# Kernel tuning notes

Hardware: AMD Instinct MI355X
Metric: run time of the kernel (lower is better)

## Reference

```python
import jax, jax.numpy as jnp
import numpy as np


def _bilinear_align_corners(img, H_out, W_out):
    # img: [B, C, h, w] -> [B, C, H_out, W_out], matching F.interpolate(mode='bilinear', align_corners=True)
    b, c, h, w = img.shape
    ys = jnp.linspace(0.0, h - 1.0, H_out)
    xs = jnp.linspace(0.0, w - 1.0, W_out)
    y0 = jnp.floor(ys).astype(jnp.int32)
    x0 = jnp.floor(xs).astype(jnp.int32)
    y1 = jnp.minimum(y0 + 1, h - 1)
    x1 = jnp.minimum(x0 + 1, w - 1)
    wy = (ys - y0)[:, None]          # [H_out, 1]
    wx = (xs - x0)[None, :]          # [1, W_out]

    def gather(yi, xi):
        return img[:, :, yi, :][:, :, :, xi]  # [B, C, H_out, W_out]

    top = gather(y0, x0) * (1.0 - wx) + gather(y0, x1) * wx
    bot = gather(y1, x0) * (1.0 - wx) + gather(y1, x1) * wx
    return top * (1.0 - wy) + bot * wy


def _conv1x1(x, W, b):
    # x: [B, C, H, W_], W: [O, C], b: [O]
    return jnp.einsum('bchw,oc->bohw', x, W) + b[None, :, None, None]


def setup_inputs() -> dict:
    key = jax.random.key(0)
    ks = jax.random.split(key, 9)
    B, C, H, W = 4, 256, 64, 64
    C8 = C // 8
    s_qk = 1.0 / np.sqrt(C)
    return {
        'x': jax.random.normal(ks[0], (B, C, H, W), dtype=jnp.float32),
        'guiding_map0': jax.random.normal(ks[1], (B, 1, 32, 32), dtype=jnp.float32),
        'Wq': jax.random.normal(ks[2], (C8, C), dtype=jnp.float32) * s_qk,
        'bq': jax.random.normal(ks[3], (C8,), dtype=jnp.float32) * 0.01,
        'Wk': jax.random.normal(ks[4], (C8, C), dtype=jnp.float32) * s_qk,
        'bk': jax.random.normal(ks[5], (C8,), dtype=jnp.float32) * 0.01,
        'Wv': jax.random.normal(ks[6], (C, C), dtype=jnp.float32) * s_qk,
        'bv': jax.random.normal(ks[7], (C,), dtype=jnp.float32) * 0.01,
        'gamma': jax.random.normal(ks[8], (1,), dtype=jnp.float32) * 0.1,
    }


def reference(x, guiding_map0, Wq, bq, Wk, bk, Wv, bv, gamma):
    B, C, H, W = x.shape
    N = H * W
    # upsample guiding map to x's spatial size, then sigmoid gate
    gm = jax.nn.sigmoid(_bilinear_align_corners(guiding_map0, H, W))  # [B,1,H,W]
    gate = 1.0 + gm

    q = (_conv1x1(x, Wq, bq) * gate).reshape(B, -1, N)  # [B, C//8, N]
    k = (_conv1x1(x, Wk, bk) * gate).reshape(B, -1, N)  # [B, C//8, N]
    v = (_conv1x1(x, Wv, bv) * gate).reshape(B, C, N)   # [B, C, N]

    # energy[b, n, m] = q[b, :, n] . k[b, :, m]
    energy = jnp.einsum('bcn,bcm->bnm', q, k)           # [B, N, N]
    attention = jax.nn.softmax(energy, axis=-1)
    # out[b, c, n] = sum_m v[b, c, m] * attention[b, n, m]
    out = jnp.einsum('bcm,bnm->bcn', v, attention).reshape(B, C, H, W)
    return gamma[0] * out + x
```

## Files before the change

### kernel.cpp

```cpp
#include <hip/hip_runtime.h>
#include <hip/hip_bf16.h>
#include <cstdint>

typedef __attribute__((ext_vector_type(4)))  float f32x4;
typedef __attribute__((ext_vector_type(16))) float f32x16;
typedef __attribute__((ext_vector_type(8)))  short s16x8;

#define LOG2E 1.4426950408889634f
#define MFIX  64.0f

#define B_   4
#define C_   256
#define N_   4096
#define NT_  256
#define MB_  128
#define QG_  128

#define WS_WFRAG 0u
#define WS_BIAS  163840u
#define WS_Q     262144u
#define WS_K     1310720u
#define WS_V     2359296u
#define WS_PART  11534336u
#define WS_ML    45088768u
#define WS_NEED  45613056ull

__device__ __forceinline__ short bf16s(float f) {
  return (short)__bfloat16_as_ushort(__float2bfloat16(f));
}
__device__ __forceinline__ float bf2f(short h) {
  union { unsigned u; float f; } v; v.u = ((unsigned)(unsigned short)h) << 16;
  return v.f;
}
__device__ __forceinline__ void gl_lds16(const void* g, void* l) {
  __builtin_amdgcn_global_load_lds(
      (const __attribute__((address_space(1))) unsigned int*)g,
      (__attribute__((address_space(3))) unsigned int*)l, 16, 0, 0);
}

__global__ void wprep_kernel(const float* __restrict__ Wq, const float* __restrict__ Wk,
                             const float* __restrict__ Wv, const float* __restrict__ bq,
                             const float* __restrict__ bk, const float* __restrict__ bv,
                             short* __restrict__ wfrag, float* __restrict__ bias) {
  int d0 = blockIdx.x * 256 + threadIdx.x;
  int d = d0;
  int j  = d & 7;  d >>= 3;
  int c  = d & 15; d >>= 4;
  int g  = d & 3;  d >>= 2;
  int ks = d & 7;  d >>= 3;
  int t  = d;
  int o  = t * 16 + c;
  int ch = ks * 32 + g * 8 + j;
  float w = (o < 32) ? Wq[o * 256 + ch] : (o < 64) ? Wk[(o - 32) * 256 + ch]
                                                   : Wv[(o - 64) * 256 + ch];
  wfrag[d0] = bf16s(w);
  if (d0 < 320) bias[d0] = (d0 < 32) ? bq[d0] : (d0 < 64) ? bk[d0 - 32] : bv[d0 - 64];
}

__global__ __launch_bounds__(256) void proj_kernel(
    const float* __restrict__ x, const short* __restrict__ wfrag,
    const float* __restrict__ bias, const float* __restrict__ gm,
    short* __restrict__ qs, short* __restrict__ ksz, short* __restrict__ vs) {
  int b = blockIdx.x >> 8, nt = blockIdx.x & 255;
  int lane = threadIdx.x & 63, wave = threadIdx.x >> 6;
  int g = lane >> 4, c = lane & 15;
  int n = nt * 16 + c;

  float gt;
  {
    int y = n >> 6, xp = n & 63;
    float fy = (float)(y * 31) / 63.0f;
    float fx = (float)(xp * 31) / 63.0f;
    int y0 = (int)fy, x0 = (int)fx;
    float wy = fy - (float)y0, wx = fx - (float)x0;
    int y1 = min(y0 + 1, 31), x1 = min(x0 + 1, 31);
    const float* p = gm + b * 1024;
    float v00 = p[y0 * 32 + x0], v01 = p[y0 * 32 + x1];
    float v10 = p[y1 * 32 + x0], v11 = p[y1 * 32 + x1];
    float top = v00 * (1.f - wx) + v01 * wx;
    float bot = v10 * (1.f - wx) + v11 * wx;
    float gv  = top * (1.f - wy) + bot * wy;
    gt = 1.0f + 1.0f / (1.0f + expf(-gv));
  }

  const float* xb = x + b * (C_ * N_) + n;
  s16x8 xf[8];
  #pragma unroll
  for (int ks = 0; ks < 8; ++ks) {
    int ch0 = ks * 32 + g * 8;
    s16x8 v;
    #pragma unroll
    for (int j = 0; j < 8; ++j) v[j] = bf16s(xb[(ch0 + j) * N_]);
    xf[ks] = v;
  }

  int qt32 = n >> 5, r = n & 31;
  for (int t = wave * 5; t < wave * 5 + 5; ++t) {
    f32x4 acc = {0.f, 0.f, 0.f, 0.f};
    #pragma unroll
    for (int ks = 0; ks < 8; ++ks) {
      s16x8 wf = *(const s16x8*)(wfrag + ((((t * 8 + ks) * 4 + g) * 16 + c) * 8));
      acc = __builtin_amdgcn_mfma_f32_16x16x32_bf16(wf, xf[ks], acc, 0, 0, 0);
    }
    #pragma unroll
    for (int jj = 0; jj < 4; ++jj) {
      int o = t * 16 + g * 4 + jj;
      float val = (acc[jj] + bias[o]) * gt;
      short bv16 = bf16s(val);
      if (o < 64) {
        int ch = o & 31;
        int s  = (ch >> 4) & 1, hi = (ch >> 3) & 1, j = ch & 7;
        short* dst = (o < 32) ? qs : ksz;
        dst[(((b * QG_ + qt32) * 2 + s) * 64 + hi * 32 + r) * 8 + j] = bv16;
      } else {
        int cv = o - 64;
        int ct = cv >> 5, lam = cv & 31;
        int s  = (r >> 4) & 1, r4 = r & 15;
        int k  = (r4 & 3) | (((r4 >> 3) & 1) << 2) | (((r4 >> 2) & 1) << 3);
        int hi = k >> 3, j = k & 7;
        vs[((((size_t)(b * MB_ + qt32) * 8 + ct) * 2 + s) * 64 + hi * 32 + lam) * 8 + j] = bv16;
      }
    }
  }
}

__global__ __launch_bounds__(512, 2) void attn_split_kernel(
    const short* __restrict__ qs, const short* __restrict__ ksz,
    const short* __restrict__ vs, short* __restrict__ part,
    float* __restrict__ mlbuf) {
  __shared__ __align__(16) short k_lds[3][1024];
  __shared__ __align__(16) short v_lds[3][8192];

  int bid = blockIdx.x;
  int b  = (bid & 7) >> 1;
  int u  = ((bid >> 3) << 1) | (bid & 1);
  int qb = u >> 2, s = u & 3;
  int tid = threadIdx.x, lane = tid & 63, wave = tid >> 6;
  int lq = lane & 31, hi = lane >> 5;
  int qt = qb * 8 + wave;

  const short* qbp = qs + (size_t)(((b * QG_ + qt) * 2) * 64 + lane) * 8;
  s16x8 qf0 = *(const s16x8*)(qbp);
  s16x8 qf1 = *(const s16x8*)(qbp + 512);
  asm volatile("s_waitcnt vmcnt(0)" ::: "memory");

  f32x16 acc[8];
  #pragma unroll
  for (int ct = 0; ct < 8; ++ct)
    #pragma unroll
    for (int e = 0; e < 16; ++e) acc[ct][e] = 0.f;
  float lsum = 0.f;

  const char* kbase = (const char*)(ksz + (size_t)b * (MB_ * 1024));
  const char* vbase = (const char*)(vs + (size_t)b * ((size_t)MB_ * 8192));

  #define STAGE(mb, nb)                                                          \
    {                                                                            \
      const char* vsrc = vbase + (size_t)(mb) * 16384;                           \
      gl_lds16(vsrc + (wave * 2 + 0) * 1024 + lane * 16,                         \
               &v_lds[nb][(wave * 2 + 0) * 512]);                                \
      gl_lds16(vsrc + (wave * 2 + 1) * 1024 + lane * 16,                         \
               &v_lds[nb][(wave * 2 + 1) * 512]);                                \
      if (wave < 2) {                                                            \
        const char* ksrc = kbase + (size_t)(mb) * 2048;                          \
        gl_lds16(ksrc + wave * 1024 + lane * 16, &k_lds[nb][wave * 512]);        \
      }                                                                          \
    }
  #define WAIT_PREV()                                                            \
    {                                                                            \
      if (wave < 2) asm volatile("s_waitcnt vmcnt(3)" ::: "memory");             \
      else          asm volatile("s_waitcnt vmcnt(2)" ::: "memory");             \
    }

  s16x8 pf0, pf1;
  f32x16 st;

  #define QKT(buf)                                                               \
    {                                                                            \
      const short* kb = k_lds[buf];                                              \
      s16x8 kf0 = *(const s16x8*)(kb + lane * 8);                                \
      s16x8 kf1 = *(const s16x8*)(kb + 512 + lane * 8);                          \
      _Pragma("unroll")                                                          \
      for (int e = 0; e < 16; ++e) st[e] = 0.f;                                  \
      st = __builtin_amdgcn_mfma_f32_32x32x16_bf16(kf0, qf0, st, 0, 0, 0);       \
      st = __builtin_amdgcn_mfma_f32_32x32x16_bf16(kf1, qf1, st, 0, 0, 0);       \
    }

  #define SOFTMAX()                                                              \
    {                                                                            \
      float psum = 0.f;                                                          \
      _Pragma("unroll")                                                          \
      for (int j = 0; j < 8; ++j) {                                              \
        float p = exp2f((st[j] - MFIX) * LOG2E);                                 \
        psum += p; pf0[j] = bf16s(p);                                            \
      }                                                                          \
      _Pragma("unroll")                                                          \
      for (int j = 0; j < 8; ++j) {                                              \
        float p = exp2f((st[8 + j] - MFIX) * LOG2E);                             \
        psum += p; pf1[j] = bf16s(p);                                            \
      }                                                                          \
      lsum += psum;                                                              \
    }

  #define PVACC(buf)                                                             \
    {                                                                            \
      const short* vb = v_lds[buf];                                              \
      _Pragma("unroll")                                                          \
      for (int ct = 0; ct < 8; ++ct) {                                           \
        s16x8 vf0 = *(const s16x8*)(vb + (ct * 2 + 0) * 512 + lane * 8);         \
        s16x8 vf1 = *(const s16x8*)(vb + (ct * 2 + 1) * 512 + lane * 8);         \
        acc[ct] = __builtin_amdgcn_mfma_f32_32x32x16_bf16(vf0, pf0, acc[ct], 0, 0, 0); \
        acc[ct] = __builtin_amdgcn_mfma_f32_32x32x16_bf16(vf1, pf1, acc[ct], 0, 0, 0); \
      }                                                                          \
    }

  STAGE(s * 32 + 0, 0);
  STAGE(s * 32 + 1, 1);
  WAIT_PREV();
  __builtin_amdgcn_s_barrier();
  QKT(0);
  SOFTMAX();

  int bc = 0, bn = 1, bs = 2;
  for (int j = 0; j < 32; ++j) {
    __builtin_amdgcn_s_barrier();
    int jn = j + 2; if (jn > 31) jn = 31;
    STAGE(s * 32 + jn, bs);
    WAIT_PREV();
    __builtin_amdgcn_s_barrier();
    __builtin_amdgcn_s_setprio(1);
    if (j < 31) QKT(bn);
    PVACC(bc);
    __builtin_amdgcn_s_setprio(0);
    if (j < 31) SOFTMAX();
    int t = bc; bc = bn; bn = bs; bs = t;
  }

  lsum += __shfl_xor(lsum, 32);

  int pt = (b * 128 + qt) * 4 + s;
  if (lane < 32) mlbuf[pt * 64 + lq] = lsum;
  short* pb = part + (size_t)pt * 8192;
  #pragma unroll
  for (int ct = 0; ct < 8; ++ct)
    #pragma unroll
    for (int e = 0; e < 16; ++e) {
      int CH = ct * 32 + (e & 3) + 8 * (e >> 2) + 4 * hi;
      pb[CH * 32 + lq] = bf16s(acc[ct][e]);
    }
  #undef STAGE
  #undef WAIT_PREV
  #undef QKT
  #undef SOFTMAX
  #undef PVACC
}

__global__ __launch_bounds__(256) void combine_kernel(
    const short* __restrict__ part, const float* __restrict__ mlbuf,
    const float* __restrict__ x, const float* __restrict__ gamma,
    float* __restrict__ out) {
  int bid = blockIdx.x;
  int b = bid >> 7, qt = bid & 127;
  int t = threadIdx.x;
  int q = t & 31, cg = t >> 5;
  int base = (b * 128 + qt) * 4;
  float L = mlbuf[(base + 0) * 64 + q] + mlbuf[(base + 1) * 64 + q]
          + mlbuf[(base + 2) * 64 + q] + mlbuf[(base + 3) * 64 + q];
  float rn = gamma[0] / L;
  int n = qt * 32 + q;
  const short* p0 = part + (size_t)(base + 0) * 8192;
  const short* p1 = part + (size_t)(base + 1) * 8192;
  const short* p2 = part + (size_t)(base + 2) * 8192;
  const short* p3 = part + (size_t)(base + 3) * 8192;
  #pragma unroll 4
  for (int cc = 0; cc < 32; ++cc) {
    int ch = cg * 32 + cc;
    int off = ch * 32 + q;
    float o = bf2f(p0[off]) + bf2f(p1[off]) + bf2f(p2[off]) + bf2f(p3[off]);
    int idx = (b * C_ + ch) * N_ + n;
    out[idx] = rn * o + x[idx];
  }
}

__global__ __launch_bounds__(256, 2) void attn_reg_kernel(
    const short* __restrict__ qs, const short* __restrict__ ksz,
    const short* __restrict__ vs, const float* __restrict__ x,
    const float* __restrict__ gamma, float* __restrict__ out) {
  __shared__ float comb_l[4][32];
  __shared__ float sumbuf[4][16][4][64];

  int bid = blockIdx.x;
  int b  = (bid & 7) >> 1;
  int qg = ((bid >> 3) << 1) | (bid & 1);
  int tid = threadIdx.x, lane = tid & 63, wave = tid >> 6;
  int lq = lane & 31;

  const short* qb = qs + (size_t)(((b * QG_ + qg) * 2) * 64 + lane) * 8;
  s16x8 qf0 = *(const s16x8*)(qb);
  s16x8 qf1 = *(const s16x8*)(qb + 512);

  f32x16 acc[8];
  #pragma unroll
  for (int ct = 0; ct < 8; ++ct)
    #pragma unroll
    for (int e = 0; e < 16; ++e) acc[ct][e] = 0.f;
  float lsum = 0.f;

  const short* kb0 = ksz + (size_t)b * (MB_ * 1024) + lane * 8;
  const short* vb0 = vs  + (size_t)b * ((size_t)MB_ * 8192) + lane * 8;

  int mb = wave;
  s16x8 kf0 = *(const s16x8*)(kb0 + mb * 1024);
  s16x8 kf1 = *(const s16x8*)(kb0 + mb * 1024 + 512);

  for (int i = 0; i < 32; ++i) {
    const short* vb = vb0 + (size_t)mb * 8192;
    s16x8 vf[16];
    #pragma unroll
    for (int t = 0; t < 16; ++t) vf[t] = *(const s16x8*)(vb + t * 512);

    f32x16 st;
    #pragma unroll
    for (int e = 0; e < 16; ++e) st[e] = 0.f;
    st = __builtin_amdgcn_mfma_f32_32x32x16_bf16(kf0, qf0, st, 0, 0, 0);
    st = __builtin_amdgcn_mfma_f32_32x32x16_bf16(kf1, qf1, st, 0, 0, 0);

    int mbn = (i < 31) ? (mb + 4) : wave;
    s16x8 nk0 = *(const s16x8*)(kb0 + mbn * 1024);
    s16x8 nk1 = *(const s16x8*)(kb0 + mbn * 1024 + 512);

    float psum = 0.f;
    s16x8 pf0, pf1;
    #pragma unroll
    for (int j = 0; j < 8; ++j) {
      float p = exp2f((st[j] - MFIX) * LOG2E);
      psum += p; pf0[j] = bf16s(p);
    }
    #pragma unroll
    for (int j = 0; j < 8; ++j) {
      float p = exp2f((st[8 + j] - MFIX) * LOG2E);
      psum += p; pf1[j] = bf16s(p);
    }
    lsum += psum;

    #pragma unroll
    for (int ct = 0; ct < 8; ++ct) {
      acc[ct] = __builtin_amdgcn_mfma_f32_32x32x16_bf16(vf[ct * 2],     pf0, acc[ct], 0, 0, 0);
      acc[ct] = __builtin_amdgcn_mfma_f32_32x32x16_bf16(vf[ct * 2 + 1], pf1, acc[ct], 0, 0, 0);
    }
    kf0 = nk0; kf1 = nk1; mb = mbn;
  }

  lsum += __shfl_xor(lsum, 32);
  if (lane < 32) comb_l[wave][lq] = lsum;
  __syncthreads();
  float L = comb_l[0][lq] + comb_l[1][lq] + comb_l[2][lq] + comb_l[3][lq];
  float rn = gamma[0] / L;
  int n = qg * 32 + lq;
  int hi = lane >> 5;

  for (int phase = 0; phase < 2; ++phase) {
    #pragma unroll
    for (int t = 0; t < 4; ++t)
      #pragma unroll
      for (int e = 0; e < 16; ++e)
        sumbuf[t][e][wave][lane] = acc[phase * 4 + t][e];
    __syncthreads();
    int ct = phase * 4 + wave;
    #pragma unroll
    for (int e = 0; e < 16; ++e) {
      float ssum = sumbuf[wave][e][0][lane] + sumbuf[wave][e][1][lane]
                 + sumbuf[wave][e][2][lane] + sumbuf[wave][e][3][lane];
      int ch = ct * 32 + (e & 3) + 8 * (e >> 2) + 4 * hi;
      int idx = (b * C_ + ch) * N_ + n;
      out[idx] = rn * ssum + x[idx];
    }
    __syncthreads();
  }
}

extern "C" void kernel_launch(void* const* d_in, const int* in_sizes, int n_in,
                              void* d_out, int out_size, void* d_ws, size_t ws_size,
                              hipStream_t stream) {
  const float* x     = (const float*)d_in[0];
  const float* gm    = (const float*)d_in[1];
  const float* Wq    = (const float*)d_in[2];
  const float* bq    = (const float*)d_in[3];
  const float* Wk    = (const float*)d_in[4];
  const float* bk    = (const float*)d_in[5];
  const float* Wv    = (const float*)d_in[6];
  const float* bv    = (const float*)d_in[7];
  const float* gamma = (const float*)d_in[8];

  char*  ws    = (char*)d_ws;
  short* wfrag = (short*)(ws + WS_WFRAG);
  float* bias  = (float*)(ws + WS_BIAS);
  short* qs    = (short*)(ws + WS_Q);
  short* ksz   = (short*)(ws + WS_K);
  short* vs    = (short*)(ws + WS_V);
  float* out   = (float*)d_out;

  wprep_kernel<<<dim3(320), dim3(256), 0, stream>>>(Wq, Wk, Wv, bq, bk, bv, wfrag, bias);
  proj_kernel<<<dim3(1024), dim3(256), 0, stream>>>(x, wfrag, bias, gm, qs, ksz, vs);

  if (ws_size >= WS_NEED) {
    short* part  = (short*)(ws + WS_PART);
    float* mlbuf = (float*)(ws + WS_ML);
    attn_split_kernel<<<dim3(256), dim3(512), 0, stream>>>(qs, ksz, vs, part, mlbuf);
    combine_kernel<<<dim3(512), dim3(256), 0, stream>>>(part, mlbuf, x, gamma, out);
  } else {
    attn_reg_kernel<<<dim3(512), dim3(256), 0, stream>>>(qs, ksz, vs, x, gamma, out);
  }
}
```

Baseline: 90.01 us.

## Split attention blocks into 4-wave blocks with 4-deep LDS ring, one barrier per step

The attention split kernel now runs 512 blocks of 256 threads, each covering four query tiles, instead of 256 blocks of 512 threads covering eight. The K/V staging ring grows from three to four LDS buffers, which drops the leading barrier in each loop iteration. The last PV accumulation is peeled out of the loop, so the per-iteration `j < 31` branches go away. Smaller blocks should synchronise more cheaply and be scheduled more flexibly. The cost is more LDS per block and twice as many K/V tile loads overall, because each block reloads the same K/V for half as many queries.

```diff
diff --git a/kernel.cpp b/kernel.cpp
--- a/kernel.cpp
+++ b/kernel.cpp
@@ -124,12 +124,12 @@
   }
 }
 
-__global__ __launch_bounds__(512, 2) void attn_split_kernel(
+__global__ __launch_bounds__(256, 2) void attn_split_kernel(
     const short* __restrict__ qs, const short* __restrict__ ksz,
     const short* __restrict__ vs, short* __restrict__ part,
     float* __restrict__ mlbuf) {
-  __shared__ __align__(16) short k_lds[3][1024];
-  __shared__ __align__(16) short v_lds[3][8192];
+  __shared__ __align__(16) short k_lds[4][1024];
+  __shared__ __align__(16) short v_lds[4][8192];
 
   int bid = blockIdx.x;
   int b  = (bid & 7) >> 1;
@@ -137,7 +137,7 @@
   int qb = u >> 2, s = u & 3;
   int tid = threadIdx.x, lane = tid & 63, wave = tid >> 6;
   int lq = lane & 31, hi = lane >> 5;
-  int qt = qb * 8 + wave;
+  int qt = qb * 4 + wave;
 
   const short* qbp = qs + (size_t)(((b * QG_ + qt) * 2) * 64 + lane) * 8;
   s16x8 qf0 = *(const s16x8*)(qbp);
@@ -157,19 +157,18 @@
   #define STAGE(mb, nb)                                                          \
     {                                                                            \
       const char* vsrc = vbase + (size_t)(mb) * 16384;                           \
-      gl_lds16(vsrc + (wave * 2 + 0) * 1024 + lane * 16,                         \
-               &v_lds[nb][(wave * 2 + 0) * 512]);                                \
-      gl_lds16(vsrc + (wave * 2 + 1) * 1024 + lane * 16,                         \
-               &v_lds[nb][(wave * 2 + 1) * 512]);                                \
-      if (wave < 2) {                                                            \
+      _Pragma("unroll")                                                          \
+      for (int r = 0; r < 4; ++r)                                                \
+        gl_lds16(vsrc + r * 4096 + tid * 16, &v_lds[nb][r * 2048 + tid * 8]);    \
+      if (tid < 128) {                                                           \
         const char* ksrc = kbase + (size_t)(mb) * 2048;                          \
-        gl_lds16(ksrc + wave * 1024 + lane * 16, &k_lds[nb][wave * 512]);        \
+        gl_lds16(ksrc + tid * 16, &k_lds[nb][tid * 8]);                          \
       }                                                                          \
     }
   #define WAIT_PREV()                                                            \
     {                                                                            \
-      if (wave < 2) asm volatile("s_waitcnt vmcnt(3)" ::: "memory");             \
-      else          asm volatile("s_waitcnt vmcnt(2)" ::: "memory");             \
+      if (wave < 2) asm volatile("s_waitcnt vmcnt(5)" ::: "memory");             \
+      else          asm volatile("s_waitcnt vmcnt(4)" ::: "memory");             \
     }
 
   s16x8 pf0, pf1;
@@ -214,27 +213,27 @@
       }                                                                          \
     }
 
-  STAGE(s * 32 + 0, 0);
-  STAGE(s * 32 + 1, 1);
-  WAIT_PREV();
-  __builtin_amdgcn_s_barrier();
-  QKT(0);
-  SOFTMAX();
-
-  int bc = 0, bn = 1, bs = 2;
-  for (int j = 0; j < 32; ++j) {
+  int base = s * 32;
+  STAGE(base + 0, 0);
+  {
+    STAGE(base + 1, 1);
+    WAIT_PREV();
     __builtin_amdgcn_s_barrier();
-    int jn = j + 2; if (jn > 31) jn = 31;
-    STAGE(s * 32 + jn, bs);
+    QKT(0);
+    SOFTMAX();
+  }
+  for (int j = 1; j < 32; ++j) {
+    int jn = (j + 1 > 31) ? 31 : j + 1;
+    STAGE(base + jn, (j + 1) & 3);
     WAIT_PREV();
     __builtin_amdgcn_s_barrier();
     __builtin_amdgcn_s_setprio(1);
-    if (j < 31) QKT(bn);
-    PVACC(bc);
+    QKT(j & 3);
+    PVACC((j - 1) & 3);
     __builtin_amdgcn_s_setprio(0);
-    if (j < 31) SOFTMAX();
-    int t = bc; bc = bn; bn = bs; bs = t;
-  }
+    SOFTMAX();
+  }
+  PVACC(31 & 3);
 
   lsum += __shfl_xor(lsum, 32);
 
@@ -406,7 +405,7 @@
   if (ws_size >= WS_NEED) {
     short* part  = (short*)(ws + WS_PART);
     float* mlbuf = (float*)(ws + WS_ML);
-    attn_split_kernel<<<dim3(256), dim3(512), 0, stream>>>(qs, ksz, vs, part, mlbuf);
+    attn_split_kernel<<<dim3(512), dim3(256), 0, stream>>>(qs, ksz, vs, part, mlbuf);
     combine_kernel<<<dim3(512), dim3(256), 0, stream>>>(part, mlbuf, x, gamma, out);
   } else {
     attn_reg_kernel<<<dim3(512), dim3(256), 0, stream>>>(qs, ksz, vs, x, gamma, out);
```

New measurement: 84.29 us. 6.4% less time.
